# Optimization experiments

Measured on AMD Instinct MI355X. Metric: run time of the kernel, lower is better.

Reference implementation:

```python
import jax, jax.numpy as jnp
import numpy as np

# Faithful JAX translation of fastmax_function with mask=True, p=1, normalize=0.
# In that branch the torch code sets temperature = 1 and uses a0 = a1 = 1.

def setup_inputs() -> dict:
    key = jax.random.key(0)
    kq, kk, kv = jax.random.split(key, 3)
    b, h, n, d = 2, 8, 8192, 32
    q = jax.random.normal(kq, (b, h, n, d), dtype=jnp.float32)
    k = jax.random.normal(kk, (b, h, n, d), dtype=jnp.float32)
    v = jax.random.normal(kv, (b, h, n, d), dtype=jnp.float32)
    return {"q": q, "k": k, "v": v}


def reference(q, k, v):
    # q, k, v: (b, h, n, d); causal (mask=True), p=1, a0=a1=1, temperature=1
    b, h, n, d = q.shape
    # first term: running sum of values
    first = jnp.cumsum(v, axis=2)                                  # (b,h,n,d)
    # second term: q_i . (sum_{j<=i} k_j v_j^T)
    kv = jnp.einsum('bhnd,bhne->bhnde', k, v)                      # (b,h,n,d,d)
    kv_cs = jnp.cumsum(kv, axis=2)                                 # (b,h,n,d,d)
    second = jnp.einsum('bhnd,bhnde->bhne', q, kv_cs)              # (b,h,n,d)
    # denominator: i + q_i . (sum_{j<=i} k_j)
    k_cs = jnp.cumsum(k, axis=2)                                   # (b,h,n,d)
    div1 = jnp.arange(1, n + 1, dtype=q.dtype)                     # (n,)
    div2 = jnp.einsum('bhnd,bhnd->bhn', q, k_cs)                   # (b,h,n)
    div = (div1[None, None, :] + div2)[..., None]                  # (b,h,n,1)
    return (first + second) / div
```

## Files before the change

### kernel.cpp

```cpp
#include <hip/hip_runtime.h>


#define D      32
#define C      64
#define NCHUNK 128
#define BH     16
#define NBLK   (BH * NCHUNK)
#define AGGU   1152

typedef __attribute__((ext_vector_type(8))) short bf16x8;
typedef __attribute__((ext_vector_type(4))) float f32x4;
typedef __attribute__((ext_vector_type(4))) unsigned short u16x4;

__device__ __forceinline__ unsigned short f2bf(float x) {
  union { float f; unsigned u; } c; c.f = x;
  unsigned r = (c.u + 0x7FFFu + ((c.u >> 16) & 1u)) >> 16;
  return (unsigned short)r;
}
__device__ __forceinline__ float bf2f(unsigned short u) {
  union { unsigned u; float f; } c; c.u = ((unsigned)u) << 16;
  return c.f;
}
__device__ __forceinline__ int permcol(int e) {
  return (e & 1) ? (16 + (e >> 1)) : (e >> 1);
}

__global__ __launch_bounds__(256) void chunk_agg_kernel(
    const float* __restrict__ k, const float* __restrict__ v,
    unsigned short* __restrict__ agg) {
  int blk = blockIdx.x;
  const float4* kp = (const float4*)k + (size_t)blk * 512;
  const float4* vp = (const float4*)v + (size_t)blk * 512;

  __shared__ __align__(16) unsigned short kT[D * 72];
  __shared__ __align__(16) unsigned short vT[D * 72];
  __shared__ __align__(16) float4 psK[256];
  __shared__ __align__(16) float4 psV[256];

  int t  = threadIdx.x;
  int j0 = t >> 3;
  int cb = (t & 7) * 4;
  int lane = t & 63, w = t >> 6;
  int m16 = lane & 15, quad = lane >> 4;
  int mb = w >> 1, nb = w & 1;
  int d1b = 16 * mb + quad * 4;
  int d2  = 16 * nb + m16;
  int n   = permcol(d2);

  float4 kA = kp[t], kB = kp[t + 256];
  float4 vA = vp[t], vB = vp[t + 256];

  {
    const float* ka = &kA.x; const float* kb = &kB.x;
    const float* va = &vA.x; const float* vb = &vB.x;
#pragma unroll
    for (int cc = 0; cc < 4; ++cc) {
      kT[(cb + cc) * 72 + j0]      = f2bf(ka[cc]);
      kT[(cb + cc) * 72 + j0 + 32] = f2bf(kb[cc]);
      vT[(cb + cc) * 72 + j0]      = f2bf(va[cc]);
      vT[(cb + cc) * 72 + j0 + 32] = f2bf(vb[cc]);
    }
    psK[t] = make_float4(kA.x + kB.x, kA.y + kB.y, kA.z + kB.z, kA.w + kB.w);
    psV[t] = make_float4(vA.x + vB.x, vA.y + vB.y, vA.z + vB.z, vA.w + vB.w);
  }
  __syncthreads();

  f32x4 acc = {0.f, 0.f, 0.f, 0.f};
#pragma unroll
  for (int kb2 = 0; kb2 < 2; ++kb2) {
    bf16x8 a = *(const bf16x8*)&kT[(16 * mb + m16) * 72 + kb2 * 32 + quad * 8];
    bf16x8 b = *(const bf16x8*)&vT[(16 * nb + m16) * 72 + kb2 * 32 + quad * 8];
    acc = __builtin_amdgcn_mfma_f32_16x16x32_bf16(a, b, acc, 0, 0, 0);
  }

  unsigned short* ap = agg + (size_t)blk * AGGU;
  *(u16x4*)&ap[n * 32 + d1b] =
      (u16x4){f2bf(acc[0]), f2bf(acc[1]), f2bf(acc[2]), f2bf(acc[3])};
  if (t < 64) {
    int ee = t & 31;
    const float* ps = (t < 32) ? (const float*)psK : (const float*)psV;
    float csum = 0.f;
#pragma unroll
    for (int m = 0; m < 32; ++m) csum += ps[ee + 32 * m];
    ((float*)(ap + 1024))[t] = csum;
  }
}

__global__ __launch_bounds__(256, 4) void output_kernel(
    const float* __restrict__ q, const float* __restrict__ k,
    const float* __restrict__ v, const unsigned short* __restrict__ agg,
    float* __restrict__ out) {
  int blk = blockIdx.x;
  int c   = blk & 127;
  int bh  = blk >> 7;
  size_t off = (size_t)blk * (C * D);
  const float4* qp4 = (const float4*)q + (size_t)blk * 512;
  const float4* kp4 = (const float4*)k + (size_t)blk * 512;
  const float4* vp4 = (const float4*)v + (size_t)blk * 512;
  const unsigned short* abh = agg + (size_t)(bh * NCHUNK) * AGGU;

  __shared__ __align__(16) char uA[10240];
  unsigned short* qbf = (unsigned short*)uA;
  unsigned short* kbf = (unsigned short*)(uA + 5120);
  float* q_s = (float*)uA;
  __shared__ __align__(16) unsigned short vTbf[D * 72];
  __shared__ __align__(16) unsigned short kvTbf[D * 40];
  __shared__ __align__(16) unsigned short Tbf[C * 72];
  __shared__ __align__(16) float kc_s[C * 36];
  __shared__ __align__(16) float gtot[8 * 32];
  __shared__ __align__(16) float pre_s[64];
  __shared__ __align__(16) float invdiv_s[C];

  int t  = threadIdx.x;
  int j0 = t >> 3;
  int cb = (t & 7) * 4;

  float4 qA = qp4[t], qB = qp4[t + 256];
  float4 kA = kp4[t], kB = kp4[t + 256];
  float4 vA = vp4[t], vB = vp4[t + 256];

  float s0 = 0.f, s1 = 0.f, s2 = 0.f, s3 = 0.f;
  float tf = 0.f;
  for (int p0 = 0; p0 < c; p0 += 8) {
    uint2 r[8]; float tl[8];
#pragma unroll
    for (int u = 0; u < 8; ++u) {
      int p = p0 + u;
      const unsigned short* apx = abh + (size_t)(p < c ? p : 0) * AGGU;
      r[u] = *(const uint2*)&apx[4 * t];
      if (t < 64) tl[u] = ((const float*)(apx + 1024))[t];
    }
#pragma unroll
    for (int u = 0; u < 8; ++u) {
      if (p0 + u < c) {
        s0 += bf2f((unsigned short)(r[u].x & 0xffff));
        s1 += bf2f((unsigned short)(r[u].x >> 16));
        s2 += bf2f((unsigned short)(r[u].y & 0xffff));
        s3 += bf2f((unsigned short)(r[u].y >> 16));
        if (t < 64) tf += tl[u];
      }
    }
  }

  for (int z = t; z < (C * 72) / 8; z += 256)
    ((uint4*)Tbf)[z] = make_uint4(0, 0, 0, 0);

  *(float4*)&kc_s[j0 * 36 + cb]        = kA;
  *(float4*)&kc_s[(j0 + 32) * 36 + cb] = kB;
  *(u16x4*)&qbf[j0 * 40 + cb] =
      (u16x4){f2bf(qA.x), f2bf(qA.y), f2bf(qA.z), f2bf(qA.w)};
  *(u16x4*)&qbf[(j0 + 32) * 40 + cb] =
      (u16x4){f2bf(qB.x), f2bf(qB.y), f2bf(qB.z), f2bf(qB.w)};
  *(u16x4*)&kbf[j0 * 40 + cb] =
      (u16x4){f2bf(kA.x), f2bf(kA.y), f2bf(kA.z), f2bf(kA.w)};
  *(u16x4*)&kbf[(j0 + 32) * 40 + cb] =
      (u16x4){f2bf(kB.x), f2bf(kB.y), f2bf(kB.z), f2bf(kB.w)};
  {
    const float* va = &vA.x; const float* vb = &vB.x;
#pragma unroll
    for (int cc = 0; cc < 4; ++cc) {
      int n = permcol(cb + cc);
      vTbf[n * 72 + j0]      = f2bf(va[cc]);
      vTbf[n * 72 + j0 + 32] = f2bf(vb[cc]);
    }
  }
  *(u16x4*)&kvTbf[(t >> 3) * 40 + (t & 7) * 4] =
      (u16x4){f2bf(s0), f2bf(s1), f2bf(s2), f2bf(s3)};
  if (t < 64) pre_s[t] = tf;
  __syncthreads();

  int lane = t & 63, w = t >> 6;
  int m16 = lane & 15, quad = lane >> 4;

  const bf16x8 aQ = *(const bf16x8*)&qbf[(16 * w + m16) * 40 + quad * 8];
  for (int jb = 0; jb <= w; ++jb) {
    bf16x8 bK = *(const bf16x8*)&kbf[(16 * jb + m16) * 40 + quad * 8];
    f32x4 cS = {0.f, 0.f, 0.f, 0.f};
    cS = __builtin_amdgcn_mfma_f32_16x16x32_bf16(aQ, bK, cS, 0, 0, 0);
    int jcol = 16 * jb + m16;
#pragma unroll
    for (int reg = 0; reg < 4; ++reg) {
      int i = 16 * w + quad * 4 + reg;
      float tv = (jcol <= i) ? (1.f + cS[reg]) : 0.f;
      Tbf[i * 72 + jcol] = f2bf(tv);
    }
  }
  int rg = t >> 5;
  int e  = t & 31;
  float vals[8];
  {
    float run = 0.f;
#pragma unroll
    for (int r = 0; r < 8; ++r) {
      vals[r] = kc_s[(rg * 8 + r) * 36 + e];
      run += vals[r];
    }
    gtot[rg * 32 + e] = run;
  }
  __syncthreads();

  {
    float offv = pre_s[e];
    for (int g2 = 0; g2 < rg; ++g2) offv += gtot[g2 * 32 + e];
    float cacc = offv;
#pragma unroll
    for (int r = 0; r < 8; ++r) {
      cacc += vals[r];
      kc_s[(rg * 8 + r) * 36 + e] = cacc;
    }
  }
  *(float4*)&q_s[j0 * 36 + cb]        = qA;
  *(float4*)&q_s[(j0 + 32) * 36 + cb] = qB;
  __syncthreads();

  if (t < 64) {
    int i = t;
    float dp = 0.f;
#pragma unroll
    for (int d4 = 0; d4 < 8; ++d4) {
      float4 qv = *(const float4*)&q_s[i * 36 + 4 * d4];
      float4 kc = *(const float4*)&kc_s[i * 36 + 4 * d4];
      dp += qv.x * kc.x + qv.y * kc.y + qv.z * kc.z + qv.w * kc.w;
    }
    invdiv_s[i] = 1.f / ((float)(c * C + i + 1) + dp);
  }
  f32x4 o0 = {0.f, 0.f, 0.f, 0.f}, o1 = {0.f, 0.f, 0.f, 0.f};
  {
    bf16x8 b0 = *(const bf16x8*)&kvTbf[(m16)      * 40 + quad * 8];
    bf16x8 b1 = *(const bf16x8*)&kvTbf[(16 + m16) * 40 + quad * 8];
    o0 = __builtin_amdgcn_mfma_f32_16x16x32_bf16(aQ, b0, o0, 0, 0, 0);
    o1 = __builtin_amdgcn_mfma_f32_16x16x32_bf16(aQ, b1, o1, 0, 0, 0);
  }
  int kbcnt = (w >= 2) ? 2 : 1;
  for (int kb2 = 0; kb2 < kbcnt; ++kb2) {
    bf16x8 aT = *(const bf16x8*)&Tbf[(16 * w + m16) * 72 + kb2 * 32 + quad * 8];
    bf16x8 b0 = *(const bf16x8*)&vTbf[(m16)      * 72 + kb2 * 32 + quad * 8];
    bf16x8 b1 = *(const bf16x8*)&vTbf[(16 + m16) * 72 + kb2 * 32 + quad * 8];
    o0 = __builtin_amdgcn_mfma_f32_16x16x32_bf16(aT, b0, o0, 0, 0, 0);
    o1 = __builtin_amdgcn_mfma_f32_16x16x32_bf16(aT, b1, o1, 0, 0, 0);
  }
  __syncthreads();

  int e0 = 2 * m16;
#pragma unroll
  for (int reg = 0; reg < 4; ++reg) {
    int i = 16 * w + quad * 4 + reg;
    float id = invdiv_s[i];
    float2 o;
    o.x = (pre_s[32 + e0]     + o0[reg]) * id;
    o.y = (pre_s[32 + e0 + 1] + o1[reg]) * id;
    *(float2*)&out[off + (size_t)i * D + e0] = o;
  }
}

extern "C" void kernel_launch(void* const* d_in, const int* in_sizes, int n_in,
                              void* d_out, int out_size, void* d_ws, size_t ws_size,
                              hipStream_t stream) {
  const float* q = (const float*)d_in[0];
  const float* k = (const float*)d_in[1];
  const float* v = (const float*)d_in[2];
  float* out = (float*)d_out;
  unsigned short* agg = (unsigned short*)d_ws;

  chunk_agg_kernel<<<NBLK, 256, 0, stream>>>(k, v, agg);
  output_kernel<<<NBLK, 256, 0, stream>>>(q, k, v, agg, out);
}
```

Baseline: 122.0 us.

## Add hierarchical group scan to replace per-chunk linear prefix accumulation

Adds a group_scan_kernel that computes exclusive prefix sums within groups of 8 chunks plus per-group totals. The output kernel then reads its in-group prefix and sums at most 15 group totals, instead of summing up to 127 earlier chunk aggregates. This cuts the quadratic redundant global reads in the output kernel. In exchange it adds a third kernel launch, extra workspace traffic, and one more bf16 rounding of the intermediate prefix values.

```diff
diff --git a/kernel.cpp b/kernel.cpp
--- a/kernel.cpp
+++ b/kernel.cpp
@@ -4,6 +4,8 @@
 #define D      32
 #define C      64
 #define NCHUNK 128
+#define GSIZE  8
+#define NGROUP 16
 #define BH     16
 #define NBLK   (BH * NCHUNK)
 #define AGGU   1152
@@ -86,18 +88,51 @@
   }
 }
 
+__global__ __launch_bounds__(256) void group_scan_kernel(
+    const unsigned short* __restrict__ agg, unsigned short* __restrict__ pref,
+    unsigned short* __restrict__ gtot) {
+  int blk = blockIdx.x;
+  int t   = threadIdx.x;
+  const unsigned short* a0 = agg + (size_t)blk * GSIZE * AGGU;
+  unsigned short* p0 = pref + (size_t)blk * GSIZE * AGGU;
+
+  uint2 r[GSIZE]; float tl[GSIZE];
+#pragma unroll
+  for (int u = 0; u < GSIZE; ++u) {
+    r[u] = *(const uint2*)&a0[(size_t)u * AGGU + 4 * t];
+    if (t < 64) tl[u] = ((const float*)(a0 + (size_t)u * AGGU + 1024))[t];
+  }
+  float s0 = 0.f, s1 = 0.f, s2 = 0.f, s3 = 0.f, st = 0.f;
+#pragma unroll
+  for (int u = 0; u < GSIZE; ++u) {
+    *(u16x4*)&p0[(size_t)u * AGGU + 4 * t] =
+        (u16x4){f2bf(s0), f2bf(s1), f2bf(s2), f2bf(s3)};
+    if (t < 64) ((float*)(p0 + (size_t)u * AGGU + 1024))[t] = st;
+    s0 += bf2f((unsigned short)(r[u].x & 0xffff));
+    s1 += bf2f((unsigned short)(r[u].x >> 16));
+    s2 += bf2f((unsigned short)(r[u].y & 0xffff));
+    s3 += bf2f((unsigned short)(r[u].y >> 16));
+    if (t < 64) st += tl[u];
+  }
+  unsigned short* gt = gtot + (size_t)blk * AGGU;
+  *(u16x4*)&gt[4 * t] = (u16x4){f2bf(s0), f2bf(s1), f2bf(s2), f2bf(s3)};
+  if (t < 64) ((float*)(gt + 1024))[t] = st;
+}
+
 __global__ __launch_bounds__(256, 4) void output_kernel(
     const float* __restrict__ q, const float* __restrict__ k,
-    const float* __restrict__ v, const unsigned short* __restrict__ agg,
-    float* __restrict__ out) {
+    const float* __restrict__ v, const unsigned short* __restrict__ pref,
+    const unsigned short* __restrict__ gtot, float* __restrict__ out) {
   int blk = blockIdx.x;
   int c   = blk & 127;
   int bh  = blk >> 7;
+  int g   = c >> 3;
   size_t off = (size_t)blk * (C * D);
   const float4* qp4 = (const float4*)q + (size_t)blk * 512;
   const float4* kp4 = (const float4*)k + (size_t)blk * 512;
   const float4* vp4 = (const float4*)v + (size_t)blk * 512;
-  const unsigned short* abh = agg + (size_t)(bh * NCHUNK) * AGGU;
+  const unsigned short* prf = pref + (size_t)blk * AGGU;
+  const unsigned short* gtb = gtot + (size_t)(bh * NGROUP) * AGGU;
 
   __shared__ __align__(16) char uA[10240];
   unsigned short* qbf = (unsigned short*)uA;
@@ -107,7 +142,7 @@
   __shared__ __align__(16) unsigned short kvTbf[D * 40];
   __shared__ __align__(16) unsigned short Tbf[C * 72];
   __shared__ __align__(16) float kc_s[C * 36];
-  __shared__ __align__(16) float gtot[8 * 32];
+  __shared__ __align__(16) float gtot_s[8 * 32];
   __shared__ __align__(16) float pre_s[64];
   __shared__ __align__(16) float invdiv_s[C];
 
@@ -119,20 +154,26 @@
   float4 kA = kp4[t], kB = kp4[t + 256];
   float4 vA = vp4[t], vB = vp4[t + 256];
 
-  float s0 = 0.f, s1 = 0.f, s2 = 0.f, s3 = 0.f;
-  float tf = 0.f;
-  for (int p0 = 0; p0 < c; p0 += 8) {
+  uint2 rp = *(const uint2*)&prf[4 * t];
+  float tlp = 0.f;
+  if (t < 64) tlp = ((const float*)(prf + 1024))[t];
+  float s0 = bf2f((unsigned short)(rp.x & 0xffff));
+  float s1 = bf2f((unsigned short)(rp.x >> 16));
+  float s2 = bf2f((unsigned short)(rp.y & 0xffff));
+  float s3 = bf2f((unsigned short)(rp.y >> 16));
+  float tf = tlp;
+  for (int p0 = 0; p0 < g; p0 += 8) {
     uint2 r[8]; float tl[8];
 #pragma unroll
     for (int u = 0; u < 8; ++u) {
       int p = p0 + u;
-      const unsigned short* apx = abh + (size_t)(p < c ? p : 0) * AGGU;
-      r[u] = *(const uint2*)&apx[4 * t];
-      if (t < 64) tl[u] = ((const float*)(apx + 1024))[t];
+      const unsigned short* gp = gtb + (size_t)(p < g ? p : 0) * AGGU;
+      r[u] = *(const uint2*)&gp[4 * t];
+      if (t < 64) tl[u] = ((const float*)(gp + 1024))[t];
     }
 #pragma unroll
     for (int u = 0; u < 8; ++u) {
-      if (p0 + u < c) {
+      if (p0 + u < g) {
         s0 += bf2f((unsigned short)(r[u].x & 0xffff));
         s1 += bf2f((unsigned short)(r[u].x >> 16));
         s2 += bf2f((unsigned short)(r[u].y & 0xffff));
@@ -195,13 +236,13 @@
       vals[r] = kc_s[(rg * 8 + r) * 36 + e];
       run += vals[r];
     }
-    gtot[rg * 32 + e] = run;
+    gtot_s[rg * 32 + e] = run;
   }
   __syncthreads();
 
   {
     float offv = pre_s[e];
-    for (int g2 = 0; g2 < rg; ++g2) offv += gtot[g2 * 32 + e];
+    for (int g2 = 0; g2 < rg; ++g2) offv += gtot_s[g2 * 32 + e];
     float cacc = offv;
 #pragma unroll
     for (int r = 0; r < 8; ++r) {
@@ -260,8 +301,11 @@
   const float* k = (const float*)d_in[1];
   const float* v = (const float*)d_in[2];
   float* out = (float*)d_out;
-  unsigned short* agg = (unsigned short*)d_ws;
+  unsigned short* agg  = (unsigned short*)d_ws;
+  unsigned short* pref = agg  + (size_t)NBLK * AGGU;
+  unsigned short* gtot = pref + (size_t)NBLK * AGGU;
 
   chunk_agg_kernel<<<NBLK, 256, 0, stream>>>(k, v, agg);
-  output_kernel<<<NBLK, 256, 0, stream>>>(q, k, v, agg, out);
-}
+  group_scan_kernel<<<BH * NGROUP, 256, 0, stream>>>(agg, pref, gtot);
+  output_kernel<<<NBLK, 256, 0, stream>>>(q, k, v, pref, gtot, out);
+}
```

Measured after the change: 106.5 us. 12.7% less time.

## Fuse chunk aggregation and output into cooperative kernel with hierarchical prefix scan

Applied to the files above, without the earlier changes.

Replaces the two-kernel scheme with one cooperative kernel that runs three phases separated by grid syncs. First, each block processes four chunks and writes local prefix states. Next, 16 blocks scan the group totals per batch-head. Finally, each block computes outputs for its four chunks while prefetching the next chunk. This removes the O(chunks) serial prefix reload in every output block, which grew quadratically with sequence position, at the cost of grid-sync overhead, fewer blocks (512) and an extra workspace pass. A three-launch fallback covers devices without cooperative launch support.

```diff
diff --git a/kernel.cpp b/kernel.cpp
--- a/kernel.cpp
+++ b/kernel.cpp
@@ -1,11 +1,17 @@
 #include <hip/hip_runtime.h>
+#include <hip/hip_cooperative_groups.h>
+
+namespace cg = cooperative_groups;
 
 
 #define D      32
 #define C      64
 #define NCHUNK 128
+#define GSIZE  4
+#define NGROUP 32
 #define BH     16
 #define NBLK   (BH * NCHUNK)
+#define NBLOCKS (NBLK / GSIZE)
 #define AGGU   1152
 
 typedef __attribute__((ext_vector_type(8))) short bf16x8;
@@ -25,231 +31,299 @@
   return (e & 1) ? (16 + (e >> 1)) : (e >> 1);
 }
 
-__global__ __launch_bounds__(256) void chunk_agg_kernel(
-    const float* __restrict__ k, const float* __restrict__ v,
-    unsigned short* __restrict__ agg) {
-  int blk = blockIdx.x;
-  const float4* kp = (const float4*)k + (size_t)blk * 512;
-  const float4* vp = (const float4*)v + (size_t)blk * 512;
-
-  __shared__ __align__(16) unsigned short kT[D * 72];
-  __shared__ __align__(16) unsigned short vT[D * 72];
-  __shared__ __align__(16) float4 psK[256];
-  __shared__ __align__(16) float4 psV[256];
+__global__ __launch_bounds__(256, 4) void fused_kernel(
+    const float* __restrict__ q, const float* __restrict__ k,
+    const float* __restrict__ v, unsigned short* __restrict__ pref,
+    unsigned short* __restrict__ gtot, unsigned short* __restrict__ gpre,
+    float* __restrict__ out, int phase) {
+  __shared__ __align__(16) char smem[37376];
 
   int t  = threadIdx.x;
   int j0 = t >> 3;
   int cb = (t & 7) * 4;
   int lane = t & 63, w = t >> 6;
   int m16 = lane & 15, quad = lane >> 4;
-  int mb = w >> 1, nb = w & 1;
-  int d1b = 16 * mb + quad * 4;
-  int d2  = 16 * nb + m16;
-  int n   = permcol(d2);
-
-  float4 kA = kp[t], kB = kp[t + 256];
-  float4 vA = vp[t], vB = vp[t + 256];
-
-  {
-    const float* ka = &kA.x; const float* kb = &kB.x;
-    const float* va = &vA.x; const float* vb = &vB.x;
-#pragma unroll
-    for (int cc = 0; cc < 4; ++cc) {
-      kT[(cb + cc) * 72 + j0]      = f2bf(ka[cc]);
-      kT[(cb + cc) * 72 + j0 + 32] = f2bf(kb[cc]);
-      vT[(cb + cc) * 72 + j0]      = f2bf(va[cc]);
-      vT[(cb + cc) * 72 + j0 + 32] = f2bf(vb[cc]);
+
+  if (phase <= 1) {
+    unsigned short* kT = (unsigned short*)smem;
+    unsigned short* vT = (unsigned short*)(smem + 4608);
+    float* psK = (float*)(smem + 9216);
+    float* psV = (float*)(smem + 13312);
+
+    int mb = w >> 1, nb = w & 1;
+    int d1b = 16 * mb + quad * 4;
+    int np  = permcol(16 * nb + m16);
+
+    int c0 = blockIdx.x * GSIZE;
+    const float4* kp = (const float4*)k + (size_t)c0 * 512;
+    const float4* vp = (const float4*)v + (size_t)c0 * 512;
+
+    float pr[4] = {0.f, 0.f, 0.f, 0.f};
+    float tailpref = 0.f;
+
+    float4 kA = kp[t], kB = kp[t + 256];
+    float4 vA = vp[t], vB = vp[t + 256];
+
+    for (int ci = 0; ci < GSIZE; ++ci) {
+      {
+        const float* ka = &kA.x; const float* kb = &kB.x;
+        const float* va = &vA.x; const float* vb = &vB.x;
+#pragma unroll
+        for (int cc = 0; cc < 4; ++cc) {
+          kT[(cb + cc) * 72 + j0]      = f2bf(ka[cc]);
+          kT[(cb + cc) * 72 + j0 + 32] = f2bf(kb[cc]);
+          vT[(cb + cc) * 72 + j0]      = f2bf(va[cc]);
+          vT[(cb + cc) * 72 + j0 + 32] = f2bf(vb[cc]);
+        }
+        *(float4*)&psK[4 * t] =
+            make_float4(kA.x + kB.x, kA.y + kB.y, kA.z + kB.z, kA.w + kB.w);
+        *(float4*)&psV[4 * t] =
+            make_float4(vA.x + vB.x, vA.y + vB.y, vA.z + vB.z, vA.w + vB.w);
+      }
+      __syncthreads();
+
+      if (ci + 1 < GSIZE) {
+        const float4* kn = kp + (size_t)(ci + 1) * 512;
+        const float4* vn = vp + (size_t)(ci + 1) * 512;
+        kA = kn[t]; kB = kn[t + 256];
+        vA = vn[t]; vB = vn[t + 256];
+      }
+
+      f32x4 acc = {0.f, 0.f, 0.f, 0.f};
+#pragma unroll
+      for (int kb2 = 0; kb2 < 2; ++kb2) {
+        bf16x8 a = *(const bf16x8*)&kT[(16 * mb + m16) * 72 + kb2 * 32 + quad * 8];
+        bf16x8 b = *(const bf16x8*)&vT[(16 * nb + m16) * 72 + kb2 * 32 + quad * 8];
+        acc = __builtin_amdgcn_mfma_f32_16x16x32_bf16(a, b, acc, 0, 0, 0);
+      }
+      float csum = 0.f;
+      if (t < 64) {
+        int ee = t & 31;
+        const float* ps = (t < 32) ? psK : psV;
+#pragma unroll
+        for (int m = 0; m < 32; ++m) csum += ps[ee + 32 * m];
+      }
+
+      unsigned short* pc = pref + (size_t)(c0 + ci) * AGGU;
+      *(u16x4*)&pc[np * 32 + d1b] =
+          (u16x4){f2bf(pr[0]), f2bf(pr[1]), f2bf(pr[2]), f2bf(pr[3])};
+#pragma unroll
+      for (int reg = 0; reg < 4; ++reg) pr[reg] += acc[reg];
+      if (t < 64) {
+        ((float*)(pc + 1024))[t] = tailpref;
+        tailpref += csum;
+      }
+      __syncthreads();
     }
-    psK[t] = make_float4(kA.x + kB.x, kA.y + kB.y, kA.z + kB.z, kA.w + kB.w);
-    psV[t] = make_float4(vA.x + vB.x, vA.y + vB.y, vA.z + vB.z, vA.w + vB.w);
-  }
-  __syncthreads();
-
-  f32x4 acc = {0.f, 0.f, 0.f, 0.f};
-#pragma unroll
-  for (int kb2 = 0; kb2 < 2; ++kb2) {
-    bf16x8 a = *(const bf16x8*)&kT[(16 * mb + m16) * 72 + kb2 * 32 + quad * 8];
-    bf16x8 b = *(const bf16x8*)&vT[(16 * nb + m16) * 72 + kb2 * 32 + quad * 8];
-    acc = __builtin_amdgcn_mfma_f32_16x16x32_bf16(a, b, acc, 0, 0, 0);
-  }
-
-  unsigned short* ap = agg + (size_t)blk * AGGU;
-  *(u16x4*)&ap[n * 32 + d1b] =
-      (u16x4){f2bf(acc[0]), f2bf(acc[1]), f2bf(acc[2]), f2bf(acc[3])};
-  if (t < 64) {
-    int ee = t & 31;
-    const float* ps = (t < 32) ? (const float*)psK : (const float*)psV;
-    float csum = 0.f;
-#pragma unroll
-    for (int m = 0; m < 32; ++m) csum += ps[ee + 32 * m];
-    ((float*)(ap + 1024))[t] = csum;
-  }
-}
-
-__global__ __launch_bounds__(256, 4) void output_kernel(
-    const float* __restrict__ q, const float* __restrict__ k,
-    const float* __restrict__ v, const unsigned short* __restrict__ agg,
-    float* __restrict__ out) {
-  int blk = blockIdx.x;
-  int c   = blk & 127;
-  int bh  = blk >> 7;
-  size_t off = (size_t)blk * (C * D);
-  const float4* qp4 = (const float4*)q + (size_t)blk * 512;
-  const float4* kp4 = (const float4*)k + (size_t)blk * 512;
-  const float4* vp4 = (const float4*)v + (size_t)blk * 512;
-  const unsigned short* abh = agg + (size_t)(bh * NCHUNK) * AGGU;
-
-  __shared__ __align__(16) char uA[10240];
-  unsigned short* qbf = (unsigned short*)uA;
-  unsigned short* kbf = (unsigned short*)(uA + 5120);
-  float* q_s = (float*)uA;
-  __shared__ __align__(16) unsigned short vTbf[D * 72];
-  __shared__ __align__(16) unsigned short kvTbf[D * 40];
-  __shared__ __align__(16) unsigned short Tbf[C * 72];
-  __shared__ __align__(16) float kc_s[C * 36];
-  __shared__ __align__(16) float gtot[8 * 32];
-  __shared__ __align__(16) float pre_s[64];
-  __shared__ __align__(16) float invdiv_s[C];
-
-  int t  = threadIdx.x;
-  int j0 = t >> 3;
-  int cb = (t & 7) * 4;
-
-  float4 qA = qp4[t], qB = qp4[t + 256];
-  float4 kA = kp4[t], kB = kp4[t + 256];
-  float4 vA = vp4[t], vB = vp4[t + 256];
-
-  float s0 = 0.f, s1 = 0.f, s2 = 0.f, s3 = 0.f;
-  float tf = 0.f;
-  for (int p0 = 0; p0 < c; p0 += 8) {
-    uint2 r[8]; float tl[8];
-#pragma unroll
-    for (int u = 0; u < 8; ++u) {
-      int p = p0 + u;
-      const unsigned short* apx = abh + (size_t)(p < c ? p : 0) * AGGU;
-      r[u] = *(const uint2*)&apx[4 * t];
-      if (t < 64) tl[u] = ((const float*)(apx + 1024))[t];
-    }
-#pragma unroll
-    for (int u = 0; u < 8; ++u) {
-      if (p0 + u < c) {
+
+    unsigned short* gt = gtot + (size_t)blockIdx.x * AGGU;
+    *(u16x4*)&gt[np * 32 + d1b] =
+        (u16x4){f2bf(pr[0]), f2bf(pr[1]), f2bf(pr[2]), f2bf(pr[3])};
+    if (t < 64) ((float*)(gt + 1024))[t] = tailpref;
+  }
+
+  if (phase == 0) cg::this_grid().sync();
+
+  if ((phase == 0 || phase == 2) && blockIdx.x < BH) {
+    const unsigned short* g0 = gtot + (size_t)blockIdx.x * NGROUP * AGGU;
+    unsigned short* p0 = gpre + (size_t)blockIdx.x * NGROUP * AGGU;
+    float s0 = 0.f, s1 = 0.f, s2 = 0.f, s3 = 0.f, st = 0.f;
+    for (int b = 0; b < NGROUP; b += 8) {
+      uint2 r[8]; float tl[8];
+#pragma unroll
+      for (int u = 0; u < 8; ++u) {
+        r[u] = *(const uint2*)&g0[(size_t)(b + u) * AGGU + 4 * t];
+        if (t < 64) tl[u] = ((const float*)(g0 + (size_t)(b + u) * AGGU + 1024))[t];
+      }
+#pragma unroll
+      for (int u = 0; u < 8; ++u) {
+        *(u16x4*)&p0[(size_t)(b + u) * AGGU + 4 * t] =
+            (u16x4){f2bf(s0), f2bf(s1), f2bf(s2), f2bf(s3)};
+        if (t < 64) ((float*)(p0 + (size_t)(b + u) * AGGU + 1024))[t] = st;
         s0 += bf2f((unsigned short)(r[u].x & 0xffff));
         s1 += bf2f((unsigned short)(r[u].x >> 16));
         s2 += bf2f((unsigned short)(r[u].y & 0xffff));
         s3 += bf2f((unsigned short)(r[u].y >> 16));
-        if (t < 64) tf += tl[u];
+        if (t < 64) st += tl[u];
       }
     }
   }
 
-  for (int z = t; z < (C * 72) / 8; z += 256)
-    ((uint4*)Tbf)[z] = make_uint4(0, 0, 0, 0);
-
-  *(float4*)&kc_s[j0 * 36 + cb]        = kA;
-  *(float4*)&kc_s[(j0 + 32) * 36 + cb] = kB;
-  *(u16x4*)&qbf[j0 * 40 + cb] =
-      (u16x4){f2bf(qA.x), f2bf(qA.y), f2bf(qA.z), f2bf(qA.w)};
-  *(u16x4*)&qbf[(j0 + 32) * 40 + cb] =
-      (u16x4){f2bf(qB.x), f2bf(qB.y), f2bf(qB.z), f2bf(qB.w)};
-  *(u16x4*)&kbf[j0 * 40 + cb] =
-      (u16x4){f2bf(kA.x), f2bf(kA.y), f2bf(kA.z), f2bf(kA.w)};
-  *(u16x4*)&kbf[(j0 + 32) * 40 + cb] =
-      (u16x4){f2bf(kB.x), f2bf(kB.y), f2bf(kB.z), f2bf(kB.w)};
-  {
-    const float* va = &vA.x; const float* vb = &vB.x;
-#pragma unroll
-    for (int cc = 0; cc < 4; ++cc) {
-      int n = permcol(cb + cc);
-      vTbf[n * 72 + j0]      = f2bf(va[cc]);
-      vTbf[n * 72 + j0 + 32] = f2bf(vb[cc]);
+  if (phase == 0) cg::this_grid().sync();
+
+  if (phase == 0 || phase == 3) {
+    unsigned short* qbf   = (unsigned short*)smem;
+    unsigned short* kbf   = (unsigned short*)(smem + 5120);
+    float*          q_s   = (float*)smem;
+    unsigned short* vTbf  = (unsigned short*)(smem + 10240);
+    unsigned short* kvTbf = (unsigned short*)(smem + 14848);
+    unsigned short* Tbf   = (unsigned short*)(smem + 17408);
+    float*          kc_s  = (float*)(smem + 26624);
+    float*          gtot_s= (float*)(smem + 35840);
+    float*          pre_s = (float*)(smem + 36864);
+    float*          invdiv_s = (float*)(smem + 37120);
+
+    int rg = t >> 5;
+    int e  = t & 31;
+
+    const unsigned short* gp = gpre + (size_t)blockIdx.x * AGGU;
+    uint2 rgp = *(const uint2*)&gp[4 * t];
+    float gtl = (t < 64) ? ((const float*)(gp + 1024))[t] : 0.f;
+    float gs0 = bf2f((unsigned short)(rgp.x & 0xffff));
+    float gs1 = bf2f((unsigned short)(rgp.x >> 16));
+    float gs2 = bf2f((unsigned short)(rgp.y & 0xffff));
+    float gs3 = bf2f((unsigned short)(rgp.y >> 16));
+    float gtf = gtl;
+
+    int blk0 = blockIdx.x * GSIZE;
+    const float4* qp4 = (const float4*)q + (size_t)blk0 * 512;
+    const float4* kp4 = (const float4*)k + (size_t)blk0 * 512;
+    const float4* vp4 = (const float4*)v + (size_t)blk0 * 512;
+    const unsigned short* prf = pref + (size_t)blk0 * AGGU;
+
+    float4 qA = qp4[t], qB = qp4[t + 256];
+    float4 kA = kp4[t], kB = kp4[t + 256];
+    float4 vA = vp4[t], vB = vp4[t + 256];
+    uint2 rp = *(const uint2*)&prf[4 * t];
+    float tlp = (t < 64) ? ((const float*)(prf + 1024))[t] : 0.f;
+
+    for (int ci = 0; ci < GSIZE; ++ci) {
+      int blk = blk0 + ci;
+      int c   = blk & 127;
+      size_t off = (size_t)blk * (C * D);
+
+      if (ci == 0) {
+        for (int z = t; z < (C * 72) / 8; z += 256)
+          ((uint4*)Tbf)[z] = make_uint4(0, 0, 0, 0);
+      }
+
+      *(float4*)&kc_s[j0 * 36 + cb]        = kA;
+      *(float4*)&kc_s[(j0 + 32) * 36 + cb] = kB;
+      *(u16x4*)&qbf[j0 * 40 + cb] =
+          (u16x4){f2bf(qA.x), f2bf(qA.y), f2bf(qA.z), f2bf(qA.w)};
+      *(u16x4*)&qbf[(j0 + 32) * 40 + cb] =
+          (u16x4){f2bf(qB.x), f2bf(qB.y), f2bf(qB.z), f2bf(qB.w)};
+      *(u16x4*)&kbf[j0 * 40 + cb] =
+          (u16x4){f2bf(kA.x), f2bf(kA.y), f2bf(kA.z), f2bf(kA.w)};
+      *(u16x4*)&kbf[(j0 + 32) * 40 + cb] =
+          (u16x4){f2bf(kB.x), f2bf(kB.y), f2bf(kB.z), f2bf(kB.w)};
+      {
+        const float* va = &vA.x; const float* vb = &vB.x;
+#pragma unroll
+        for (int cc = 0; cc < 4; ++cc) {
+          int n = permcol(cb + cc);
+          vTbf[n * 72 + j0]      = f2bf(va[cc]);
+          vTbf[n * 72 + j0 + 32] = f2bf(vb[cc]);
+        }
+      }
+      {
+        float s0 = gs0 + bf2f((unsigned short)(rp.x & 0xffff));
+        float s1 = gs1 + bf2f((unsigned short)(rp.x >> 16));
+        float s2 = gs2 + bf2f((unsigned short)(rp.y & 0xffff));
+        float s3 = gs3 + bf2f((unsigned short)(rp.y >> 16));
+        *(u16x4*)&kvTbf[(t >> 3) * 40 + (t & 7) * 4] =
+            (u16x4){f2bf(s0), f2bf(s1), f2bf(s2), f2bf(s3)};
+      }
+      if (t < 64) pre_s[t] = gtf + tlp;
+      __syncthreads();
+
+      float4 nqA = make_float4(0,0,0,0), nqB = nqA, nkA = nqA, nkB = nqA,
+             nvA = nqA, nvB = nqA;
+      uint2 nrp = make_uint2(0, 0); float ntlp = 0.f;
+      if (ci + 1 < GSIZE) {
+        const float4* qn = qp4 + (size_t)(ci + 1) * 512;
+        const float4* kn = kp4 + (size_t)(ci + 1) * 512;
+        const float4* vn = vp4 + (size_t)(ci + 1) * 512;
+        nqA = qn[t]; nqB = qn[t + 256];
+        nkA = kn[t]; nkB = kn[t + 256];
+        nvA = vn[t]; nvB = vn[t + 256];
+        const unsigned short* pn = prf + (size_t)(ci + 1) * AGGU;
+        nrp = *(const uint2*)&pn[4 * t];
+        if (t < 64) ntlp = ((const float*)(pn + 1024))[t];
+      }
+
+      const bf16x8 aQ = *(const bf16x8*)&qbf[(16 * w + m16) * 40 + quad * 8];
+      for (int jb = 0; jb <= w; ++jb) {
+        bf16x8 bK = *(const bf16x8*)&kbf[(16 * jb + m16) * 40 + quad * 8];
+        f32x4 cS = {0.f, 0.f, 0.f, 0.f};
+        cS = __builtin_amdgcn_mfma_f32_16x16x32_bf16(aQ, bK, cS, 0, 0, 0);
+        int jcol = 16 * jb + m16;
+#pragma unroll
+        for (int reg = 0; reg < 4; ++reg) {
+          int i = 16 * w + quad * 4 + reg;
+          float tv = (jcol <= i) ? (1.f + cS[reg]) : 0.f;
+          Tbf[i * 72 + jcol] = f2bf(tv);
+        }
+      }
+      float vals[8];
+      {
+        float run = 0.f;
+#pragma unroll
+        for (int r = 0; r < 8; ++r) {
+          vals[r] = kc_s[(rg * 8 + r) * 36 + e];
+          run += vals[r];
+        }
+        gtot_s[rg * 32 + e] = run;
+      }
+      __syncthreads();
+
+      {
+        float offv = pre_s[e];
+        for (int g2 = 0; g2 < rg; ++g2) offv += gtot_s[g2 * 32 + e];
+        float cacc = offv;
+#pragma unroll
+        for (int r = 0; r < 8; ++r) {
+          cacc += vals[r];
+          kc_s[(rg * 8 + r) * 36 + e] = cacc;
+        }
+      }
+      *(float4*)&q_s[j0 * 36 + cb]        = qA;
+      *(float4*)&q_s[(j0 + 32) * 36 + cb] = qB;
+      __syncthreads();
+
+      if (t < 64) {
+        int i = t;
+        float dp = 0.f;
+#pragma unroll
+        for (int d4 = 0; d4 < 8; ++d4) {
+          float4 qv = *(const float4*)&q_s[i * 36 + 4 * d4];
+          float4 kc = *(const float4*)&kc_s[i * 36 + 4 * d4];
+          dp += qv.x * kc.x + qv.y * kc.y + qv.z * kc.z + qv.w * kc.w;
+        }
+        invdiv_s[i] = 1.f / ((float)(c * C + i + 1) + dp);
+      }
+      f32x4 o0 = {0.f, 0.f, 0.f, 0.f}, o1 = {0.f, 0.f, 0.f, 0.f};
+      {
+        bf16x8 b0 = *(const bf16x8*)&kvTbf[(m16)      * 40 + quad * 8];
+        bf16x8 b1 = *(const bf16x8*)&kvTbf[(16 + m16) * 40 + quad * 8];
+        o0 = __builtin_amdgcn_mfma_f32_16x16x32_bf16(aQ, b0, o0, 0, 0, 0);
+        o1 = __builtin_amdgcn_mfma_f32_16x16x32_bf16(aQ, b1, o1, 0, 0, 0);
+      }
+      int kbcnt = (w >= 2) ? 2 : 1;
+      for (int kb2 = 0; kb2 < kbcnt; ++kb2) {
+        bf16x8 aT = *(const bf16x8*)&Tbf[(16 * w + m16) * 72 + kb2 * 32 + quad * 8];
+        bf16x8 b0 = *(const bf16x8*)&vTbf[(m16)      * 72 + kb2 * 32 + quad * 8];
+        bf16x8 b1 = *(const bf16x8*)&vTbf[(16 + m16) * 72 + kb2 * 32 + quad * 8];
+        o0 = __builtin_amdgcn_mfma_f32_16x16x32_bf16(aT, b0, o0, 0, 0, 0);
+        o1 = __builtin_amdgcn_mfma_f32_16x16x32_bf16(aT, b1, o1, 0, 0, 0);
+      }
+      __syncthreads();
+
+      int e0 = 2 * m16;
+#pragma unroll
+      for (int reg = 0; reg < 4; ++reg) {
+        int i = 16 * w + quad * 4 + reg;
+        float id = invdiv_s[i];
+        float2 o;
+        o.x = (pre_s[32 + e0]     + o0[reg]) * id;
+        o.y = (pre_s[32 + e0 + 1] + o1[reg]) * id;
+        *(float2*)&out[off + (size_t)i * D + e0] = o;
+      }
+      __syncthreads();
+
+      qA = nqA; qB = nqB; kA = nkA; kB = nkB; vA = nvA; vB = nvB;
+      rp = nrp; tlp = ntlp;
     }
-  }
-  *(u16x4*)&kvTbf[(t >> 3) * 40 + (t & 7) * 4] =
-      (u16x4){f2bf(s0), f2bf(s1), f2bf(s2), f2bf(s3)};
-  if (t < 64) pre_s[t] = tf;
-  __syncthreads();
-
-  int lane = t & 63, w = t >> 6;
-  int m16 = lane & 15, quad = lane >> 4;
-
-  const bf16x8 aQ = *(const bf16x8*)&qbf[(16 * w + m16) * 40 + quad * 8];
-  for (int jb = 0; jb <= w; ++jb) {
-    bf16x8 bK = *(const bf16x8*)&kbf[(16 * jb + m16) * 40 + quad * 8];
-    f32x4 cS = {0.f, 0.f, 0.f, 0.f};
-    cS = __builtin_amdgcn_mfma_f32_16x16x32_bf16(aQ, bK, cS, 0, 0, 0);
-    int jcol = 16 * jb + m16;
-#pragma unroll
-    for (int reg = 0; reg < 4; ++reg) {
-      int i = 16 * w + quad * 4 + reg;
-      float tv = (jcol <= i) ? (1.f + cS[reg]) : 0.f;
-      Tbf[i * 72 + jcol] = f2bf(tv);
-    }
-  }
-  int rg = t >> 5;
-  int e  = t & 31;
-  float vals[8];
-  {
-    float run = 0.f;
-#pragma unroll
-    for (int r = 0; r < 8; ++r) {
-      vals[r] = kc_s[(rg * 8 + r) * 36 + e];
-      run += vals[r];
-    }
-    gtot[rg * 32 + e] = run;
-  }
-  __syncthreads();
-
-  {
-    float offv = pre_s[e];
-    for (int g2 = 0; g2 < rg; ++g2) offv += gtot[g2 * 32 + e];
-    float cacc = offv;
-#pragma unroll
-    for (int r = 0; r < 8; ++r) {
-      cacc += vals[r];
-      kc_s[(rg * 8 + r) * 36 + e] = cacc;
-    }
-  }
-  *(float4*)&q_s[j0 * 36 + cb]        = qA;
-  *(float4*)&q_s[(j0 + 32) * 36 + cb] = qB;
-  __syncthreads();
-
-  if (t < 64) {
-    int i = t;
-    float dp = 0.f;
-#pragma unroll
-    for (int d4 = 0; d4 < 8; ++d4) {
-      float4 qv = *(const float4*)&q_s[i * 36 + 4 * d4];
-      float4 kc = *(const float4*)&kc_s[i * 36 + 4 * d4];
-      dp += qv.x * kc.x + qv.y * kc.y + qv.z * kc.z + qv.w * kc.w;
-    }
-    invdiv_s[i] = 1.f / ((float)(c * C + i + 1) + dp);
-  }
-  f32x4 o0 = {0.f, 0.f, 0.f, 0.f}, o1 = {0.f, 0.f, 0.f, 0.f};
-  {
-    bf16x8 b0 = *(const bf16x8*)&kvTbf[(m16)      * 40 + quad * 8];
-    bf16x8 b1 = *(const bf16x8*)&kvTbf[(16 + m16) * 40 + quad * 8];
-    o0 = __builtin_amdgcn_mfma_f32_16x16x32_bf16(aQ, b0, o0, 0, 0, 0);
-    o1 = __builtin_amdgcn_mfma_f32_16x16x32_bf16(aQ, b1, o1, 0, 0, 0);
-  }
-  int kbcnt = (w >= 2) ? 2 : 1;
-  for (int kb2 = 0; kb2 < kbcnt; ++kb2) {
-    bf16x8 aT = *(const bf16x8*)&Tbf[(16 * w + m16) * 72 + kb2 * 32 + quad * 8];
-    bf16x8 b0 = *(const bf16x8*)&vTbf[(m16)      * 72 + kb2 * 32 + quad * 8];
-    bf16x8 b1 = *(const bf16x8*)&vTbf[(16 + m16) * 72 + kb2 * 32 + quad * 8];
-    o0 = __builtin_amdgcn_mfma_f32_16x16x32_bf16(aT, b0, o0, 0, 0, 0);
-    o1 = __builtin_amdgcn_mfma_f32_16x16x32_bf16(aT, b1, o1, 0, 0, 0);
-  }
-  __syncthreads();
-
-  int e0 = 2 * m16;
-#pragma unroll
-  for (int reg = 0; reg < 4; ++reg) {
-    int i = 16 * w + quad * 4 + reg;
-    float id = invdiv_s[i];
-    float2 o;
-    o.x = (pre_s[32 + e0]     + o0[reg]) * id;
-    o.y = (pre_s[32 + e0 + 1] + o1[reg]) * id;
-    *(float2*)&out[off + (size_t)i * D + e0] = o;
   }
 }
 
@@ -260,8 +334,34 @@
   const float* k = (const float*)d_in[1];
   const float* v = (const float*)d_in[2];
   float* out = (float*)d_out;
-  unsigned short* agg = (unsigned short*)d_ws;
-
-  chunk_agg_kernel<<<NBLK, 256, 0, stream>>>(k, v, agg);
-  output_kernel<<<NBLK, 256, 0, stream>>>(q, k, v, agg, out);
-}
+  unsigned short* pref = (unsigned short*)d_ws;
+  unsigned short* gtot = pref + (size_t)NBLK * AGGU;
+  unsigned short* gpre = gtot + (size_t)NBLOCKS * AGGU;
+
+  static int coop_ok = -1;
+  if (coop_ok < 0) {
+    int dev = 0;
+    (void)hipGetDevice(&dev);
+    int attr = 0;
+    (void)hipDeviceGetAttribute(&attr, hipDeviceAttributeCooperativeLaunch, dev);
+    int perCU = 0;
+    (void)hipOccupancyMaxActiveBlocksPerMultiprocessor(&perCU, fused_kernel, 256, 0);
+    int ncu = 0;
+    (void)hipDeviceGetAttribute(&ncu, hipDeviceAttributeMultiprocessorCount, dev);
+    coop_ok = (attr != 0 && (long)perCU * ncu >= NBLOCKS) ? 1 : 0;
+  }
+
+  if (coop_ok == 1) {
+    int phase = 0;
+    void* args[] = {(void*)&q, (void*)&k, (void*)&v, (void*)&pref,
+                    (void*)&gtot, (void*)&gpre, (void*)&out, (void*)&phase};
+    hipError_t err = hipLaunchCooperativeKernel(
+        fused_kernel, dim3(NBLOCKS), dim3(256), args, 0, stream);
+    if (err == hipSuccess) return;
+    coop_ok = 0;
+  }
+
+  fused_kernel<<<NBLOCKS, 256, 0, stream>>>(q, k, v, pref, gtot, gpre, out, 1);
+  fused_kernel<<<BH,      256, 0, stream>>>(q, k, v, pref, gtot, gpre, out, 2);
+  fused_kernel<<<NBLOCKS, 256, 0, stream>>>(q, k, v, pref, gtot, gpre, out, 3);
+}
```

New measurement: 236.9 us. 94.2% more time.
